# Kernel tuning notes

Hardware: AMD Instinct MI355X
Metric: run time of the kernel (lower is better)

Reference implementation:

```python
import jax, jax.numpy as jnp
import numpy as np

N_NODES = 50000
N_EDGES = 800000
H = 128   # atom_hidden_feats
B = 64    # bond_in_feats
NEG_SLOPE = 0.01  # torch LeakyReLU default


def setup_inputs() -> dict:
    key = jax.random.key(0)
    k1, k2, k3, k4, k5 = jax.random.split(key, 5)
    feat = jax.random.normal(k1, (N_NODES, H), dtype=jnp.float32)
    gdf_feat = jax.random.normal(k2, (N_EDGES, B), dtype=jnp.float32)
    # Linear(2H+B -> H): weight [H, 2H+B], bias [H]
    W = jax.random.normal(k3, (H, 2 * H + B), dtype=jnp.float32) * 0.05
    b = jnp.zeros((H,), dtype=jnp.float32)
    src = jax.random.randint(k4, (N_EDGES,), 0, N_NODES, dtype=jnp.int64)
    dst = jax.random.randint(k5, (N_EDGES,), 0, N_NODES, dtype=jnp.int64)
    return {"feat": feat, "gdf_feat": gdf_feat, "W": W, "b": b, "src": src, "dst": dst}


def reference(feat, gdf_feat, W, b, src, dst):
    n_nodes = feat.shape[0]
    # Per-edge message: concat(src_feat, dst_feat, edge_feat) -> linear -> gate
    z = jnp.concatenate([feat[src], feat[dst], gdf_feat], axis=-1)  # [E, 2H+B]
    z = z @ W.T + b                                                 # [E, H]
    msg = jax.nn.sigmoid(z) * jnp.where(z > 0, z, NEG_SLOPE * z)    # sigmoid * leaky_relu
    # Scatter-sum messages to destination nodes
    return jax.ops.segment_sum(msg, dst, num_segments=n_nodes)      # [N, H]
```

## Files before the change

### kernel.cpp

```cpp
#include <hip/hip_runtime.h>
#include <hip/hip_bf16.h>

typedef __attribute__((ext_vector_type(8)))  short bf16x8;
typedef __attribute__((ext_vector_type(16))) float f32x16;
typedef __attribute__((ext_vector_type(4)))  float f32x4;
typedef __attribute__((ext_vector_type(2)))  __fp16 fp16x2;

#define NN 50000
#define EE 800000
#define HH 128
#define KK 320
#define NEG 0.01f
#define NTILES (EE / 64)
#define NBLK 768
#define ACC_BYTES ((size_t)NN * HH * 2)

__device__ __forceinline__ unsigned pack2(float a, float b) {
    unsigned short lo = __builtin_bit_cast(unsigned short, __float2bfloat16(a));
    unsigned short hi = __builtin_bit_cast(unsigned short, __float2bfloat16(b));
    return (unsigned)lo | ((unsigned)hi << 16);
}

__global__ __launch_bounds__(256) void featcvt_kernel(const float* __restrict__ feat,
                                                      ushort* __restrict__ featb)
{
    const int t = blockIdx.x * 256 + threadIdx.x;
    const float* p = feat + (long long)t * 8;
    f32x4 v0 = *(const f32x4*)p;
    f32x4 v1 = *(const f32x4*)(p + 4);
    int4 h;
    h.x = (int)pack2(v0[0], v0[1]); h.y = (int)pack2(v0[2], v0[3]);
    h.z = (int)pack2(v1[0], v1[1]); h.w = (int)pack2(v1[2], v1[3]);
    *(int4*)(featb + (long long)t * 8) = h;
}

__global__ __launch_bounds__(256, 3) void fused_pipe_kernel(
    const ushort* __restrict__ featb, const float* __restrict__ gdf,
    const float*  __restrict__ W,     const float* __restrict__ bias,
    const int*    __restrict__ src,   const int*   __restrict__ dst,
    __fp16* __restrict__ acc16)
{
    __shared__ char lds[64 * 640];
    __shared__ int  dsts[2][64];

    const int tid  = threadIdx.x;
    const int lane = tid & 63;
    const int wid  = tid >> 6;
    const int col  = wid * 32 + (lane & 31);
    const int khalf = lane >> 5;
    const int r = tid >> 2, q = tid & 3;

    bf16x8 Wb[20];
    {
        const float* wrow = W + col * KK + khalf * 8;
        #pragma unroll
        for (int k = 0; k < 20; k++) {
            f32x4 x0 = *(const f32x4*)(wrow + k * 16);
            f32x4 x1 = *(const f32x4*)(wrow + k * 16 + 4);
            union { bf16x8 v; unsigned u[4]; } t;
            t.u[0] = pack2(x0[0], x0[1]); t.u[1] = pack2(x0[2], x0[3]);
            t.u[2] = pack2(x1[0], x1[1]); t.u[3] = pack2(x1[2], x1[3]);
            Wb[k] = t.v;
        }
    }
    const float bv = bias[col];

    int4  sf[8];
    f32x4 sgv[4];
    int   dStage;

    auto issueLoads = [&](long long t, int s_i, int d_i) {
        const ushort* fs = featb + (long long)s_i * HH;
        const ushort* fd = featb + (long long)d_i * HH;
        const float*  ge = gdf + (t * 64 + r) * 64;
        #pragma unroll
        for (int i = 0; i < 8; i++) {
            const int c = q + i * 4;
            sf[i] = *(const int4*)((c < 16) ? (fs + c * 8) : (fd + (c - 16) * 8));
        }
        #pragma unroll
        for (int i = 0; i < 2; i++) {
            const int cg = q + i * 4;
            sgv[2 * i]     = *(const f32x4*)(ge + cg * 8);
            sgv[2 * i + 1] = *(const f32x4*)(ge + cg * 8 + 4);
        }
    };
    auto writeStage = [&](int buf) {
        const int xr = (r & 7) << 4;
        #pragma unroll
        for (int i = 0; i < 8; i++) {
            const int c = q + i * 4;
            *(int4*)(lds + r * 640 + ((c * 16) ^ xr)) = sf[i];
        }
        #pragma unroll
        for (int i = 0; i < 2; i++) {
            const int c = 32 + q + i * 4;
            int4 h;
            h.x = (int)pack2(sgv[2*i][0], sgv[2*i][1]);
            h.y = (int)pack2(sgv[2*i][2], sgv[2*i][3]);
            h.z = (int)pack2(sgv[2*i+1][0], sgv[2*i+1][1]);
            h.w = (int)pack2(sgv[2*i+1][2], sgv[2*i+1][3]);
            *(int4*)(lds + r * 640 + ((c * 16) ^ xr)) = h;
        }
        if (q == 0) dsts[buf][r] = dStage;
    };

    int tile = blockIdx.x;
    {
        int s0 = src[(long long)tile * 64 + r];
        int d0 = dst[(long long)tile * 64 + r];
        issueLoads(tile, s0, d0);
        dStage = d0;
    }
    int nt = tile + NBLK;
    int sN, dN;
    {
        const long long tc = (nt < NTILES) ? nt : 0;
        sN = src[tc * 64 + r]; dN = dst[tc * 64 + r];
    }
    writeStage(0);
    asm volatile("s_waitcnt lgkmcnt(0)" ::: "memory");
    __builtin_amdgcn_sched_barrier(0);
    __builtin_amdgcn_s_barrier();

    const int arow = lane & 31;
    const int xa   = (arow & 7) << 4;
    int cur = 0;

    while (true) {
        const bool hasNext = (nt < NTILES);
        if (hasNext) {
            issueLoads(nt, sN, dN);
            dStage = dN;
            const long long tc = (nt + NBLK < NTILES) ? (long long)(nt + NBLK) : 0;
            sN = src[tc * 64 + r]; dN = dst[tc * 64 + r];
        }

        f32x16 acc0 = {}; f32x16 acc1 = {};
        #pragma unroll
        for (int k = 0; k < 20; k++) {
            const int kb = k * 32 + khalf * 16;
            bf16x8 a0 = *(const bf16x8*)(lds + arow * 640 + (kb ^ xa));
            bf16x8 a1 = *(const bf16x8*)(lds + (arow + 32) * 640 + (kb ^ xa));
            acc0 = __builtin_amdgcn_mfma_f32_32x32x16_bf16(a0, Wb[k], acc0, 0, 0, 0);
            acc1 = __builtin_amdgcn_mfma_f32_32x32x16_bf16(a1, Wb[k], acc1, 0, 0, 0);
        }

        if (hasNext) {
            __builtin_amdgcn_s_barrier();
            __builtin_amdgcn_sched_barrier(0);
            writeStage(cur ^ 1);
            asm volatile("s_waitcnt lgkmcnt(0)" ::: "memory");
            __builtin_amdgcn_sched_barrier(0);
            __builtin_amdgcn_s_barrier();
        }

        #pragma unroll
        for (int rt = 0; rt < 2; rt++) {
            const f32x16 A = rt ? acc1 : acc0;
            #pragma unroll
            for (int g = 0; g < 4; g++) {
                const int4 dn4 = *(const int4*)(&dsts[cur][rt * 32 + g * 8 + khalf * 4]);
                #pragma unroll
                for (int j = 0; j < 4; j++) {
                    const int reg = g * 4 + j;
                    const float z  = A[reg] + bv;
                    const float lr = z > 0.f ? z : NEG * z;
                    const float sgm = 1.f / (1.f + __expf(-z));
                    const float m  = lr * sgm;
                    const float o  = __shfl_xor(m, 1);
                    const int dn = ((const int*)&dn4)[j];
                    if (!(lane & 1)) {
                        fp16x2 hv = __builtin_amdgcn_cvt_pkrtz(m, o);
                        __fp16* p = acc16 + (long long)dn * HH + col;
                        asm volatile("global_atomic_pk_add_f16 %0, %1, off"
                                     :: "v"(p), "v"(hv) : "memory");
                    }
                }
            }
        }

        if (!hasNext) break;
        cur ^= 1; tile = nt; nt += NBLK;
    }
}

__global__ __launch_bounds__(256) void fused_fallback_kernel(
    const float* __restrict__ feat, const float* __restrict__ gdf,
    const float* __restrict__ W,    const float* __restrict__ bias,
    const int*   __restrict__ src,  const int*   __restrict__ dst,
    float* __restrict__ out)
{
    __shared__ int4 lds4[64 * 40];
    __shared__ int  dsts[64];
    char* lds = (char*)lds4;
    const int tid = threadIdx.x, lane = tid & 63, wid = tid >> 6;
    const int col = wid * 32 + (lane & 31), khalf = lane >> 5;
    const int r = tid >> 2, q = tid & 3;
    const long long ebase = (long long)blockIdx.x * 64;

    bf16x8 Wb[20];
    {
        const float* wrow = W + col * KK + khalf * 8;
        #pragma unroll
        for (int k = 0; k < 20; k++) {
            f32x4 x0 = *(const f32x4*)(wrow + k * 16);
            f32x4 x1 = *(const f32x4*)(wrow + k * 16 + 4);
            union { bf16x8 v; unsigned u[4]; } t;
            t.u[0] = pack2(x0[0], x0[1]); t.u[1] = pack2(x0[2], x0[3]);
            t.u[2] = pack2(x1[0], x1[1]); t.u[3] = pack2(x1[2], x1[3]);
            Wb[k] = t.v;
        }
    }
    const int s = src[ebase + r], d = dst[ebase + r];
    if (q == 0) dsts[r] = d;
    {
        const float* fs = feat + (long long)s * HH;
        const float* fd = feat + (long long)d * HH;
        const float* ge = gdf + (ebase + r) * 64;
        #pragma unroll
        for (int i = 0; i < 10; i++) {
            const int c = q + i * 4;
            const float* p = (c < 16) ? (fs + c * 8)
                           : (c < 32) ? (fd + (c - 16) * 8)
                                      : (ge + (c - 32) * 8);
            f32x4 v0 = *(const f32x4*)p;
            f32x4 v1 = *(const f32x4*)(p + 4);
            int4 h;
            h.x = (int)pack2(v0[0], v0[1]); h.y = (int)pack2(v0[2], v0[3]);
            h.z = (int)pack2(v1[0], v1[1]); h.w = (int)pack2(v1[2], v1[3]);
            *(int4*)(lds + r * 640 + ((c * 16) ^ ((r & 7) << 4))) = h;
        }
    }
    __syncthreads();
    f32x16 acc0 = {}; f32x16 acc1 = {};
    const int arow = lane & 31, xa = (arow & 7) << 4;
    #pragma unroll
    for (int k = 0; k < 20; k++) {
        const int kb = k * 32 + khalf * 16;
        bf16x8 a0 = *(const bf16x8*)(lds + arow * 640 + (kb ^ xa));
        bf16x8 a1 = *(const bf16x8*)(lds + (arow + 32) * 640 + (kb ^ xa));
        acc0 = __builtin_amdgcn_mfma_f32_32x32x16_bf16(a0, Wb[k], acc0, 0, 0, 0);
        acc1 = __builtin_amdgcn_mfma_f32_32x32x16_bf16(a1, Wb[k], acc1, 0, 0, 0);
    }
    const float bv = bias[col];
    #pragma unroll
    for (int rt = 0; rt < 2; rt++) {
        const f32x16 A = rt ? acc1 : acc0;
        #pragma unroll
        for (int g = 0; g < 4; g++) {
            #pragma unroll
            for (int j = 0; j < 4; j++) {
                const int reg = g * 4 + j;
                const int row = j + g * 8 + khalf * 4;
                const float z  = A[reg] + bv;
                const float lr = z > 0.f ? z : NEG * z;
                const float sgm = 1.f / (1.f + __expf(-z));
                unsafeAtomicAdd(out + (long long)dsts[rt * 32 + row] * HH + col, lr * sgm);
            }
        }
    }
}

__global__ __launch_bounds__(256) void conv_kernel(const int4* __restrict__ acc,
                                                   float4* __restrict__ out)
{
    const int i = blockIdx.x * 256 + threadIdx.x;
    union { int4 v; __fp16 h[8]; } u;
    u.v = acc[i];
    float4 a, b;
    a.x = (float)u.h[0]; a.y = (float)u.h[1]; a.z = (float)u.h[2]; a.w = (float)u.h[3];
    b.x = (float)u.h[4]; b.y = (float)u.h[5]; b.z = (float)u.h[6]; b.w = (float)u.h[7];
    out[2 * i]     = a;
    out[2 * i + 1] = b;
}

extern "C" void kernel_launch(void* const* d_in, const int* in_sizes, int n_in,
                              void* d_out, int out_size, void* d_ws, size_t ws_size,
                              hipStream_t stream) {
    const float* feat = (const float*)d_in[0];
    const float* gdf  = (const float*)d_in[1];
    const float* W    = (const float*)d_in[2];
    const float* bias = (const float*)d_in[3];
    const int*   src  = (const int*)d_in[4];
    const int*   dst  = (const int*)d_in[5];
    float* out = (float*)d_out;

    __fp16* acc16 = (__fp16*)d_ws;
    ushort* featb = (ushort*)((char*)d_ws + ACC_BYTES);

    if (ws_size >= 2 * ACC_BYTES) {
        (void)hipMemsetAsync(d_ws, 0, ACC_BYTES, stream);
        featcvt_kernel<<<NN * HH / 8 / 256, 256, 0, stream>>>(feat, featb);
        fused_pipe_kernel<<<NBLK, 256, 0, stream>>>(featb, gdf, W, bias,
                                                    src, dst, acc16);
        conv_kernel<<<NN * HH / 8 / 256, 256, 0, stream>>>((const int4*)d_ws,
                                                           (float4*)out);
    } else {
        (void)hipMemsetAsync(out, 0, (size_t)out_size * sizeof(float), stream);
        fused_fallback_kernel<<<EE / 64, 256, 0, stream>>>(feat, gdf, W, bias,
                                                           src, dst, out);
    }
}
```

Measured before the change: 371.2 us.

## Replace atomic scatter with counting-sort slots and segmented reduction

Builds a destination histogram, prefix scan and per-edge slot assignment, so each edge's fp16 message is written to a unique slot in a dst-sorted buffer instead of being atomically added. A separate reduce kernel then sums each node's contiguous messages into fp32 output. This removes global packed fp16 atomics and the conversion pass. In exchange it needs about 200MB of workspace, several extra kernel launches, and extra message write/read traffic. If the workspace is too small it falls back to the old atomic path.

```diff
diff --git a/kernel.cpp b/kernel.cpp
--- a/kernel.cpp
+++ b/kernel.cpp
@@ -13,7 +13,13 @@
 #define NEG 0.01f
 #define NTILES (EE / 64)
 #define NBLK 768
-#define ACC_BYTES ((size_t)NN * HH * 2)
+#define NSB 196
+
+#define MSG_BYTES   ((size_t)EE * HH * 2)
+#define FEATB_BYTES ((size_t)NN * HH * 2)
+#define SLOT_BYTES  ((size_t)EE * 4)
+#define CNT_BYTES   ((size_t)50176 * 4)
+#define ACC_BYTES   ((size_t)NN * HH * 2)
 
 __device__ __forceinline__ unsigned pack2(float a, float b) {
     unsigned short lo = __builtin_bit_cast(unsigned short, __float2bfloat16(a));
@@ -34,14 +40,75 @@
     *(int4*)(featb + (long long)t * 8) = h;
 }
 
-__global__ __launch_bounds__(256, 3) void fused_pipe_kernel(
+__global__ __launch_bounds__(256) void hist_kernel(const int* __restrict__ dst,
+                                                   unsigned* __restrict__ cnt)
+{
+    const int e = blockIdx.x * 256 + threadIdx.x;
+    atomicAdd(&cnt[dst[e]], 1u);
+}
+
+__global__ __launch_bounds__(256) void scan1_kernel(const unsigned* __restrict__ cnt,
+                                                    unsigned* __restrict__ base,
+                                                    unsigned* __restrict__ bsum)
+{
+    __shared__ unsigned s[256];
+    const int tid = threadIdx.x;
+    const int g = blockIdx.x * 256 + tid;
+    unsigned v = (g < NN) ? cnt[g] : 0u;
+    s[tid] = v; __syncthreads();
+    #pragma unroll
+    for (int o = 1; o < 256; o <<= 1) {
+        unsigned t = (tid >= o) ? s[tid - o] : 0u;
+        __syncthreads();
+        if (tid >= o) s[tid] += t;
+        __syncthreads();
+    }
+    if (g < NN) base[g] = s[tid] - v;
+    if (tid == 255) bsum[blockIdx.x] = s[255];
+}
+
+__global__ __launch_bounds__(256) void scan2_kernel(unsigned* __restrict__ bsum)
+{
+    __shared__ unsigned s[256];
+    const int tid = threadIdx.x;
+    unsigned v = (tid < NSB) ? bsum[tid] : 0u;
+    s[tid] = v; __syncthreads();
+    #pragma unroll
+    for (int o = 1; o < 256; o <<= 1) {
+        unsigned t = (tid >= o) ? s[tid - o] : 0u;
+        __syncthreads();
+        if (tid >= o) s[tid] += t;
+        __syncthreads();
+    }
+    if (tid < NSB) bsum[tid] = s[tid] - v;
+}
+
+__global__ __launch_bounds__(256) void scan3_kernel(unsigned* __restrict__ base,
+                                                    const unsigned* __restrict__ bsum)
+{
+    const int g = blockIdx.x * 256 + threadIdx.x;
+    if (g < NN) base[g] += bsum[blockIdx.x];
+}
+
+__global__ __launch_bounds__(256) void slot_kernel(const int* __restrict__ dst,
+                                                   const unsigned* __restrict__ base,
+                                                   unsigned* __restrict__ cursor,
+                                                   int* __restrict__ slot)
+{
+    const int e = blockIdx.x * 256 + threadIdx.x;
+    const int d = dst[e];
+    const unsigned rank = atomicAdd(&cursor[d], 1u);
+    slot[e] = (int)(base[d] + rank);
+}
+
+__global__ __launch_bounds__(256, 3) void fused_store_kernel(
     const ushort* __restrict__ featb, const float* __restrict__ gdf,
     const float*  __restrict__ W,     const float* __restrict__ bias,
     const int*    __restrict__ src,   const int*   __restrict__ dst,
-    __fp16* __restrict__ acc16)
+    const int*    __restrict__ slot,  __fp16* __restrict__ msg)
 {
     __shared__ char lds[64 * 640];
-    __shared__ int  dsts[2][64];
+    __shared__ int  sslot[2][64];
 
     const int tid  = threadIdx.x;
     const int lane = tid & 63;
@@ -67,7 +134,7 @@
 
     int4  sf[8];
     f32x4 sgv[4];
-    int   dStage;
+    int   slStage;
 
     auto issueLoads = [&](long long t, int s_i, int d_i) {
         const ushort* fs = featb + (long long)s_i * HH;
@@ -102,6 +169,174 @@
             h.w = (int)pack2(sgv[2*i+1][2], sgv[2*i+1][3]);
             *(int4*)(lds + r * 640 + ((c * 16) ^ xr)) = h;
         }
+        if (q == 0) sslot[buf][r] = slStage;
+    };
+
+    int tile = blockIdx.x;
+    {
+        int s0 = src[(long long)tile * 64 + r];
+        int d0 = dst[(long long)tile * 64 + r];
+        issueLoads(tile, s0, d0);
+        slStage = slot[(long long)tile * 64 + r];
+    }
+    int nt = tile + NBLK;
+    int sN, dN, slN;
+    {
+        const long long tc = (nt < NTILES) ? nt : 0;
+        sN = src[tc * 64 + r]; dN = dst[tc * 64 + r]; slN = slot[tc * 64 + r];
+    }
+    writeStage(0);
+    asm volatile("s_waitcnt lgkmcnt(0)" ::: "memory");
+    __builtin_amdgcn_sched_barrier(0);
+    __builtin_amdgcn_s_barrier();
+
+    const int arow = lane & 31;
+    const int xa   = (arow & 7) << 4;
+    int cur = 0;
+
+    while (true) {
+        const bool hasNext = (nt < NTILES);
+        if (hasNext) {
+            issueLoads(nt, sN, dN);
+            slStage = slN;
+            const long long tc = (nt + NBLK < NTILES) ? (long long)(nt + NBLK) : 0;
+            sN = src[tc * 64 + r]; dN = dst[tc * 64 + r]; slN = slot[tc * 64 + r];
+        }
+
+        f32x16 acc0 = {}; f32x16 acc1 = {};
+        #pragma unroll
+        for (int k = 0; k < 20; k++) {
+            const int kb = k * 32 + khalf * 16;
+            bf16x8 a0 = *(const bf16x8*)(lds + arow * 640 + (kb ^ xa));
+            bf16x8 a1 = *(const bf16x8*)(lds + (arow + 32) * 640 + (kb ^ xa));
+            acc0 = __builtin_amdgcn_mfma_f32_32x32x16_bf16(a0, Wb[k], acc0, 0, 0, 0);
+            acc1 = __builtin_amdgcn_mfma_f32_32x32x16_bf16(a1, Wb[k], acc1, 0, 0, 0);
+        }
+
+        if (hasNext) {
+            __builtin_amdgcn_s_barrier();
+            __builtin_amdgcn_sched_barrier(0);
+            writeStage(cur ^ 1);
+            asm volatile("s_waitcnt lgkmcnt(0)" ::: "memory");
+            __builtin_amdgcn_sched_barrier(0);
+            __builtin_amdgcn_s_barrier();
+        }
+
+        #pragma unroll
+        for (int rt = 0; rt < 2; rt++) {
+            const f32x16 A = rt ? acc1 : acc0;
+            #pragma unroll
+            for (int g = 0; g < 4; g++) {
+                const int4 sl4 = *(const int4*)(&sslot[cur][rt * 32 + g * 8 + khalf * 4]);
+                #pragma unroll
+                for (int j = 0; j < 4; j++) {
+                    const int reg = g * 4 + j;
+                    const float z  = A[reg] + bv;
+                    const float lr = z > 0.f ? z : NEG * z;
+                    const float sgm = 1.f / (1.f + __expf(-z));
+                    const float m  = lr * sgm;
+                    const float o  = __shfl_xor(m, 1);
+                    const int sl = ((const int*)&sl4)[j];
+                    if (!(lane & 1)) {
+                        fp16x2 hv = __builtin_amdgcn_cvt_pkrtz(m, o);
+                        *(fp16x2*)(msg + (long long)sl * HH + col) = hv;
+                    }
+                }
+            }
+        }
+
+        if (!hasNext) break;
+        cur ^= 1; tile = nt; nt += NBLK;
+    }
+}
+
+__global__ __launch_bounds__(256) void reduce_kernel(const __fp16* __restrict__ msg,
+                                                     const unsigned* __restrict__ base,
+                                                     const unsigned* __restrict__ cnt,
+                                                     float* __restrict__ out)
+{
+    const int n    = blockIdx.x * 4 + (threadIdx.x >> 6);
+    const int lane = threadIdx.x & 63;
+    const unsigned st  = base[n];
+    const unsigned deg = cnt[n];
+    float a0 = 0.f, a1 = 0.f;
+    unsigned j = 0;
+    union { unsigned u; __fp16 h[2]; } w0, w1;
+    for (; j + 2 <= deg; j += 2) {
+        w0.u = *(const unsigned*)(msg + ((long long)(st + j)     * HH) + lane * 2);
+        w1.u = *(const unsigned*)(msg + ((long long)(st + j + 1) * HH) + lane * 2);
+        a0 += (float)w0.h[0] + (float)w1.h[0];
+        a1 += (float)w0.h[1] + (float)w1.h[1];
+    }
+    if (j < deg) {
+        w0.u = *(const unsigned*)(msg + ((long long)(st + j) * HH) + lane * 2);
+        a0 += (float)w0.h[0];
+        a1 += (float)w0.h[1];
+    }
+    *(float2*)(out + (long long)n * HH + lane * 2) = float2{a0, a1};
+}
+
+__global__ __launch_bounds__(256, 3) void fused_pipe_kernel(
+    const ushort* __restrict__ featb, const float* __restrict__ gdf,
+    const float*  __restrict__ W,     const float* __restrict__ bias,
+    const int*    __restrict__ src,   const int*   __restrict__ dst,
+    __fp16* __restrict__ acc16)
+{
+    __shared__ char lds[64 * 640];
+    __shared__ int  dsts[2][64];
+    const int tid = threadIdx.x, lane = tid & 63, wid = tid >> 6;
+    const int col = wid * 32 + (lane & 31), khalf = lane >> 5;
+    const int r = tid >> 2, q = tid & 3;
+
+    bf16x8 Wb[20];
+    {
+        const float* wrow = W + col * KK + khalf * 8;
+        #pragma unroll
+        for (int k = 0; k < 20; k++) {
+            f32x4 x0 = *(const f32x4*)(wrow + k * 16);
+            f32x4 x1 = *(const f32x4*)(wrow + k * 16 + 4);
+            union { bf16x8 v; unsigned u[4]; } t;
+            t.u[0] = pack2(x0[0], x0[1]); t.u[1] = pack2(x0[2], x0[3]);
+            t.u[2] = pack2(x1[0], x1[1]); t.u[3] = pack2(x1[2], x1[3]);
+            Wb[k] = t.v;
+        }
+    }
+    const float bv = bias[col];
+    int4 sf[8]; f32x4 sgv[4]; int dStage;
+
+    auto issueLoads = [&](long long t, int s_i, int d_i) {
+        const ushort* fs = featb + (long long)s_i * HH;
+        const ushort* fd = featb + (long long)d_i * HH;
+        const float*  ge = gdf + (t * 64 + r) * 64;
+        #pragma unroll
+        for (int i = 0; i < 8; i++) {
+            const int c = q + i * 4;
+            sf[i] = *(const int4*)((c < 16) ? (fs + c * 8) : (fd + (c - 16) * 8));
+        }
+        #pragma unroll
+        for (int i = 0; i < 2; i++) {
+            const int cg = q + i * 4;
+            sgv[2 * i]     = *(const f32x4*)(ge + cg * 8);
+            sgv[2 * i + 1] = *(const f32x4*)(ge + cg * 8 + 4);
+        }
+    };
+    auto writeStage = [&](int buf) {
+        const int xr = (r & 7) << 4;
+        #pragma unroll
+        for (int i = 0; i < 8; i++) {
+            const int c = q + i * 4;
+            *(int4*)(lds + r * 640 + ((c * 16) ^ xr)) = sf[i];
+        }
+        #pragma unroll
+        for (int i = 0; i < 2; i++) {
+            const int c = 32 + q + i * 4;
+            int4 h;
+            h.x = (int)pack2(sgv[2*i][0], sgv[2*i][1]);
+            h.y = (int)pack2(sgv[2*i][2], sgv[2*i][3]);
+            h.z = (int)pack2(sgv[2*i+1][0], sgv[2*i+1][1]);
+            h.w = (int)pack2(sgv[2*i+1][2], sgv[2*i+1][3]);
+            *(int4*)(lds + r * 640 + ((c * 16) ^ xr)) = h;
+        }
         if (q == 0) dsts[buf][r] = dStage;
     };
 
@@ -123,10 +358,8 @@
     __builtin_amdgcn_sched_barrier(0);
     __builtin_amdgcn_s_barrier();
 
-    const int arow = lane & 31;
-    const int xa   = (arow & 7) << 4;
+    const int arow = lane & 31, xa = (arow & 7) << 4;
     int cur = 0;
-
     while (true) {
         const bool hasNext = (nt < NTILES);
         if (hasNext) {
@@ -135,7 +368,6 @@
             const long long tc = (nt + NBLK < NTILES) ? (long long)(nt + NBLK) : 0;
             sN = src[tc * 64 + r]; dN = dst[tc * 64 + r];
         }
-
         f32x16 acc0 = {}; f32x16 acc1 = {};
         #pragma unroll
         for (int k = 0; k < 20; k++) {
@@ -145,7 +377,6 @@
             acc0 = __builtin_amdgcn_mfma_f32_32x32x16_bf16(a0, Wb[k], acc0, 0, 0, 0);
             acc1 = __builtin_amdgcn_mfma_f32_32x32x16_bf16(a1, Wb[k], acc1, 0, 0, 0);
         }
-
         if (hasNext) {
             __builtin_amdgcn_s_barrier();
             __builtin_amdgcn_sched_barrier(0);
@@ -154,7 +385,6 @@
             __builtin_amdgcn_sched_barrier(0);
             __builtin_amdgcn_s_barrier();
         }
-
         #pragma unroll
         for (int rt = 0; rt < 2; rt++) {
             const f32x16 A = rt ? acc1 : acc0;
@@ -179,10 +409,22 @@
                 }
             }
         }
-
         if (!hasNext) break;
         cur ^= 1; tile = nt; nt += NBLK;
     }
+}
+
+__global__ __launch_bounds__(256) void conv_kernel(const int4* __restrict__ acc,
+                                                   float4* __restrict__ out)
+{
+    const int i = blockIdx.x * 256 + threadIdx.x;
+    union { int4 v; __fp16 h[8]; } u;
+    u.v = acc[i];
+    float4 a, b;
+    a.x = (float)u.h[0]; a.y = (float)u.h[1]; a.z = (float)u.h[2]; a.w = (float)u.h[3];
+    b.x = (float)u.h[4]; b.y = (float)u.h[5]; b.z = (float)u.h[6]; b.w = (float)u.h[7];
+    out[2 * i]     = a;
+    out[2 * i + 1] = b;
 }
 
 __global__ __launch_bounds__(256) void fused_fallback_kernel(
@@ -262,19 +504,6 @@
     }
 }
 
-__global__ __launch_bounds__(256) void conv_kernel(const int4* __restrict__ acc,
-                                                   float4* __restrict__ out)
-{
-    const int i = blockIdx.x * 256 + threadIdx.x;
-    union { int4 v; __fp16 h[8]; } u;
-    u.v = acc[i];
-    float4 a, b;
-    a.x = (float)u.h[0]; a.y = (float)u.h[1]; a.z = (float)u.h[2]; a.w = (float)u.h[3];
-    b.x = (float)u.h[4]; b.y = (float)u.h[5]; b.z = (float)u.h[6]; b.w = (float)u.h[7];
-    out[2 * i]     = a;
-    out[2 * i + 1] = b;
-}
-
 extern "C" void kernel_launch(void* const* d_in, const int* in_sizes, int n_in,
                               void* d_out, int out_size, void* d_ws, size_t ws_size,
                               hipStream_t stream) {
@@ -286,13 +515,33 @@
     const int*   dst  = (const int*)d_in[5];
     float* out = (float*)d_out;
 
-    __fp16* acc16 = (__fp16*)d_ws;
-    ushort* featb = (ushort*)((char*)d_ws + ACC_BYTES);
-
-    if (ws_size >= 2 * ACC_BYTES) {
+    char* wsb = (char*)d_ws;
+    __fp16*   msg    = (__fp16*)wsb;
+    ushort*   featb  = (ushort*)(wsb + MSG_BYTES);
+    int*      slot   = (int*)(wsb + MSG_BYTES + FEATB_BYTES);
+    unsigned* cnt    = (unsigned*)(wsb + MSG_BYTES + FEATB_BYTES + SLOT_BYTES);
+    unsigned* base   = cnt + 50176;
+    unsigned* cursor = base + 50176;
+    unsigned* bsum   = cursor + 50176;
+    const size_t fullBytes = MSG_BYTES + FEATB_BYTES + SLOT_BYTES + 3 * CNT_BYTES + 1024;
+
+    if (ws_size >= fullBytes) {
+        (void)hipMemsetAsync(cnt, 0, 3 * CNT_BYTES + 1024, stream);
+        featcvt_kernel<<<NN * HH / 8 / 256, 256, 0, stream>>>(feat, featb);
+        hist_kernel<<<EE / 256, 256, 0, stream>>>(dst, cnt);
+        scan1_kernel<<<NSB, 256, 0, stream>>>(cnt, base, bsum);
+        scan2_kernel<<<1, 256, 0, stream>>>(bsum);
+        scan3_kernel<<<NSB, 256, 0, stream>>>(base, bsum);
+        slot_kernel<<<EE / 256, 256, 0, stream>>>(dst, base, cursor, slot);
+        fused_store_kernel<<<NBLK, 256, 0, stream>>>(featb, gdf, W, bias,
+                                                     src, dst, slot, msg);
+        reduce_kernel<<<NN / 4, 256, 0, stream>>>(msg, base, cnt, out);
+    } else if (ws_size >= 2 * ACC_BYTES) {
+        __fp16* acc16 = (__fp16*)d_ws;
+        ushort* fb2   = (ushort*)(wsb + ACC_BYTES);
         (void)hipMemsetAsync(d_ws, 0, ACC_BYTES, stream);
-        featcvt_kernel<<<NN * HH / 8 / 256, 256, 0, stream>>>(feat, featb);
-        fused_pipe_kernel<<<NBLK, 256, 0, stream>>>(featb, gdf, W, bias,
+        featcvt_kernel<<<NN * HH / 8 / 256, 256, 0, stream>>>(feat, fb2);
+        fused_pipe_kernel<<<NBLK, 256, 0, stream>>>(fb2, gdf, W, bias,
                                                     src, dst, acc16);
         conv_kernel<<<NN * HH / 8 / 256, 256, 0, stream>>>((const int4*)d_ws,
                                                            (float4*)out);
```

Measured after the change: 506.0 us. 1.36x slower.

## Sort edges by destination and pre-combine same-destination messages before atomics

Applied to the files above, without the earlier changes.

Adds a counting sort of edges by destination (histogram, three-stage scan, atomic permutation build). The main kernel walks contiguous sorted tile ranges per block, with XCD-aware block-to-range mapping, and sums runs of equal destinations in registers before issuing packed fp16 atomics. The aim is fewer atomics and better locality for the destination-feature gather and the scatter. In exchange it adds several preprocessing kernels per call, an indirect gather of gdf through the permutation, and it drops the register double-buffered prefetch pipeline, so loads are now synchronous with the compute.

```diff
diff --git a/kernel.cpp b/kernel.cpp
--- a/kernel.cpp
+++ b/kernel.cpp
@@ -13,7 +13,12 @@
 #define NEG 0.01f
 #define NTILES (EE / 64)
 #define NBLK 768
-#define ACC_BYTES ((size_t)NN * HH * 2)
+#define NSB 196
+
+#define ACC_BYTES   ((size_t)NN * HH * 2)
+#define FEATB_BYTES ((size_t)NN * HH * 2)
+#define PERM_BYTES  ((size_t)EE * 4)
+#define CNT_BYTES   ((size_t)50176 * 4)
 
 __device__ __forceinline__ unsigned pack2(float a, float b) {
     unsigned short lo = __builtin_bit_cast(unsigned short, __float2bfloat16(a));
@@ -34,14 +39,75 @@
     *(int4*)(featb + (long long)t * 8) = h;
 }
 
-__global__ __launch_bounds__(256, 3) void fused_pipe_kernel(
+__global__ __launch_bounds__(256) void hist_kernel(const int* __restrict__ dst,
+                                                   unsigned* __restrict__ cnt)
+{
+    const int e = blockIdx.x * 256 + threadIdx.x;
+    atomicAdd(&cnt[dst[e]], 1u);
+}
+
+__global__ __launch_bounds__(256) void scan1_kernel(const unsigned* __restrict__ cnt,
+                                                    unsigned* __restrict__ base,
+                                                    unsigned* __restrict__ bsum)
+{
+    __shared__ unsigned s[256];
+    const int tid = threadIdx.x;
+    const int g = blockIdx.x * 256 + tid;
+    unsigned v = (g < NN) ? cnt[g] : 0u;
+    s[tid] = v; __syncthreads();
+    #pragma unroll
+    for (int o = 1; o < 256; o <<= 1) {
+        unsigned t = (tid >= o) ? s[tid - o] : 0u;
+        __syncthreads();
+        if (tid >= o) s[tid] += t;
+        __syncthreads();
+    }
+    if (g < NN) base[g] = s[tid] - v;
+    if (tid == 255) bsum[blockIdx.x] = s[255];
+}
+
+__global__ __launch_bounds__(256) void scan2_kernel(unsigned* __restrict__ bsum)
+{
+    __shared__ unsigned s[256];
+    const int tid = threadIdx.x;
+    unsigned v = (tid < NSB) ? bsum[tid] : 0u;
+    s[tid] = v; __syncthreads();
+    #pragma unroll
+    for (int o = 1; o < 256; o <<= 1) {
+        unsigned t = (tid >= o) ? s[tid - o] : 0u;
+        __syncthreads();
+        if (tid >= o) s[tid] += t;
+        __syncthreads();
+    }
+    if (tid < NSB) bsum[tid] = s[tid] - v;
+}
+
+__global__ __launch_bounds__(256) void scan3_kernel(unsigned* __restrict__ base,
+                                                    const unsigned* __restrict__ bsum)
+{
+    const int g = blockIdx.x * 256 + threadIdx.x;
+    if (g < NN) base[g] += bsum[blockIdx.x];
+}
+
+__global__ __launch_bounds__(256) void permbuild_kernel(const int* __restrict__ dst,
+                                                        const unsigned* __restrict__ base,
+                                                        unsigned* __restrict__ cursor,
+                                                        int* __restrict__ perm)
+{
+    const int e = blockIdx.x * 256 + threadIdx.x;
+    const int d = dst[e];
+    const unsigned rank = atomicAdd(&cursor[d], 1u);
+    perm[base[d] + rank] = e;
+}
+
+__global__ __launch_bounds__(256, 3) void fused_sorted_kernel(
     const ushort* __restrict__ featb, const float* __restrict__ gdf,
     const float*  __restrict__ W,     const float* __restrict__ bias,
     const int*    __restrict__ src,   const int*   __restrict__ dst,
-    __fp16* __restrict__ acc16)
+    const int*    __restrict__ perm,  __fp16* __restrict__ acc16)
 {
     __shared__ char lds[64 * 640];
-    __shared__ int  dsts[2][64];
+    __shared__ int  dsts[64];
 
     const int tid  = threadIdx.x;
     const int lane = tid & 63;
@@ -65,76 +131,62 @@
     }
     const float bv = bias[col];
 
-    int4  sf[8];
-    f32x4 sgv[4];
-    int   dStage;
-
-    auto issueLoads = [&](long long t, int s_i, int d_i) {
-        const ushort* fs = featb + (long long)s_i * HH;
-        const ushort* fd = featb + (long long)d_i * HH;
-        const float*  ge = gdf + (t * 64 + r) * 64;
-        #pragma unroll
-        for (int i = 0; i < 8; i++) {
-            const int c = q + i * 4;
-            sf[i] = *(const int4*)((c < 16) ? (fs + c * 8) : (fd + (c - 16) * 8));
-        }
-        #pragma unroll
-        for (int i = 0; i < 2; i++) {
-            const int cg = q + i * 4;
-            sgv[2 * i]     = *(const f32x4*)(ge + cg * 8);
-            sgv[2 * i + 1] = *(const f32x4*)(ge + cg * 8 + 4);
-        }
-    };
-    auto writeStage = [&](int buf) {
-        const int xr = (r & 7) << 4;
-        #pragma unroll
-        for (int i = 0; i < 8; i++) {
-            const int c = q + i * 4;
-            *(int4*)(lds + r * 640 + ((c * 16) ^ xr)) = sf[i];
-        }
-        #pragma unroll
-        for (int i = 0; i < 2; i++) {
-            const int c = 32 + q + i * 4;
-            int4 h;
-            h.x = (int)pack2(sgv[2*i][0], sgv[2*i][1]);
-            h.y = (int)pack2(sgv[2*i][2], sgv[2*i][3]);
-            h.z = (int)pack2(sgv[2*i+1][0], sgv[2*i+1][1]);
-            h.w = (int)pack2(sgv[2*i+1][2], sgv[2*i+1][3]);
-            *(int4*)(lds + r * 640 + ((c * 16) ^ xr)) = h;
-        }
-        if (q == 0) dsts[buf][r] = dStage;
-    };
-
-    int tile = blockIdx.x;
+    const int xcd = blockIdx.x & 7, wI = blockIdx.x >> 3;
+    const int cid = xcd * (NBLK / 8) + wI;
+    const int qc  = NTILES / NBLK;
+    const int rem = NTILES % NBLK;
+    const int t0  = cid * qc + (cid < rem ? cid : rem);
+    const int len = qc + (cid < rem ? 1 : 0);
+
+    int eCur, sCur, dCur;
     {
-        int s0 = src[(long long)tile * 64 + r];
-        int d0 = dst[(long long)tile * 64 + r];
-        issueLoads(tile, s0, d0);
-        dStage = d0;
-    }
-    int nt = tile + NBLK;
-    int sN, dN;
-    {
-        const long long tc = (nt < NTILES) ? nt : 0;
-        sN = src[tc * 64 + r]; dN = dst[tc * 64 + r];
-    }
-    writeStage(0);
-    asm volatile("s_waitcnt lgkmcnt(0)" ::: "memory");
-    __builtin_amdgcn_sched_barrier(0);
-    __builtin_amdgcn_s_barrier();
+        const long long p = (long long)t0 * 64 + r;
+        eCur = perm[p]; sCur = src[eCur]; dCur = dst[eCur];
+    }
 
     const int arow = lane & 31;
     const int xa   = (arow & 7) << 4;
-    int cur = 0;
-
-    while (true) {
-        const bool hasNext = (nt < NTILES);
-        if (hasNext) {
-            issueLoads(nt, sN, dN);
-            dStage = dN;
-            const long long tc = (nt + NBLK < NTILES) ? (long long)(nt + NBLK) : 0;
-            sN = src[tc * 64 + r]; dN = dst[tc * 64 + r];
-        }
+
+    auto flush = [&](int dn, float v) {
+        const float o = __shfl_xor(v, 1);
+        if (!(lane & 1)) {
+            fp16x2 hv = __builtin_amdgcn_cvt_pkrtz(v, o);
+            __fp16* pa = acc16 + (long long)dn * HH + col;
+            asm volatile("global_atomic_pk_add_f16 %0, %1, off"
+                         :: "v"(pa), "v"(hv) : "memory");
+        }
+    };
+
+    for (int t = t0; t < t0 + len; ++t) {
+        if (q == 0) dsts[r] = dCur;
+        {
+            const ushort* fs = featb + (long long)sCur * HH;
+            const ushort* fd = featb + (long long)dCur * HH;
+            const float*  ge = gdf + (long long)eCur * 64;
+            const int xr = (r & 7) << 4;
+            #pragma unroll
+            for (int i = 0; i < 8; i++) {
+                const int c = q + i * 4;
+                int4 h = *(const int4*)((c < 16) ? (fs + c * 8) : (fd + (c - 16) * 8));
+                *(int4*)(lds + r * 640 + ((c * 16) ^ xr)) = h;
+            }
+            #pragma unroll
+            for (int i = 8; i < 10; i++) {
+                const int c = q + i * 4;
+                const float* p = ge + (c - 32) * 8;
+                f32x4 v0 = *(const f32x4*)p;
+                f32x4 v1 = *(const f32x4*)(p + 4);
+                int4 h;
+                h.x = (int)pack2(v0[0], v0[1]); h.y = (int)pack2(v0[2], v0[3]);
+                h.z = (int)pack2(v1[0], v1[1]); h.w = (int)pack2(v1[2], v1[3]);
+                *(int4*)(lds + r * 640 + ((c * 16) ^ xr)) = h;
+            }
+        }
+        if (t + 1 < t0 + len) {
+            const long long p = (long long)(t + 1) * 64 + r;
+            eCur = perm[p]; sCur = src[eCur]; dCur = dst[eCur];
+        }
+        __syncthreads();
 
         f32x16 acc0 = {}; f32x16 acc1 = {};
         #pragma unroll
@@ -146,43 +198,44 @@
             acc1 = __builtin_amdgcn_mfma_f32_32x32x16_bf16(a1, Wb[k], acc1, 0, 0, 0);
         }
 
-        if (hasNext) {
-            __builtin_amdgcn_s_barrier();
-            __builtin_amdgcn_sched_barrier(0);
-            writeStage(cur ^ 1);
-            asm volatile("s_waitcnt lgkmcnt(0)" ::: "memory");
-            __builtin_amdgcn_sched_barrier(0);
-            __builtin_amdgcn_s_barrier();
-        }
-
         #pragma unroll
         for (int rt = 0; rt < 2; rt++) {
             const f32x16 A = rt ? acc1 : acc0;
             #pragma unroll
             for (int g = 0; g < 4; g++) {
-                const int4 dn4 = *(const int4*)(&dsts[cur][rt * 32 + g * 8 + khalf * 4]);
+                const int4 dn4 = *(const int4*)(&dsts[rt * 32 + g * 8 + khalf * 4]);
+                const int dd[4] = { dn4.x, dn4.y, dn4.z, dn4.w };
+                float mm[4];
                 #pragma unroll
                 for (int j = 0; j < 4; j++) {
-                    const int reg = g * 4 + j;
-                    const float z  = A[reg] + bv;
+                    const float z  = A[g * 4 + j] + bv;
                     const float lr = z > 0.f ? z : NEG * z;
-                    const float sgm = 1.f / (1.f + __expf(-z));
-                    const float m  = lr * sgm;
-                    const float o  = __shfl_xor(m, 1);
-                    const int dn = ((const int*)&dn4)[j];
-                    if (!(lane & 1)) {
-                        fp16x2 hv = __builtin_amdgcn_cvt_pkrtz(m, o);
-                        __fp16* p = acc16 + (long long)dn * HH + col;
-                        asm volatile("global_atomic_pk_add_f16 %0, %1, off"
-                                     :: "v"(p), "v"(hv) : "memory");
-                    }
+                    mm[j] = lr / (1.f + __expf(-z));
                 }
+                float s = mm[0];
+                #pragma unroll
+                for (int j = 1; j < 4; j++) {
+                    if (dd[j] == dd[j - 1]) s += mm[j];
+                    else { flush(dd[j - 1], s); s = mm[j]; }
+                }
+                flush(dd[3], s);
             }
         }
-
-        if (!hasNext) break;
-        cur ^= 1; tile = nt; nt += NBLK;
-    }
+        __syncthreads();
+    }
+}
+
+__global__ __launch_bounds__(256) void conv_kernel(const int4* __restrict__ acc,
+                                                   float4* __restrict__ out)
+{
+    const int i = blockIdx.x * 256 + threadIdx.x;
+    union { int4 v; __fp16 h[8]; } u;
+    u.v = acc[i];
+    float4 a, b;
+    a.x = (float)u.h[0]; a.y = (float)u.h[1]; a.z = (float)u.h[2]; a.w = (float)u.h[3];
+    b.x = (float)u.h[4]; b.y = (float)u.h[5]; b.z = (float)u.h[6]; b.w = (float)u.h[7];
+    out[2 * i]     = a;
+    out[2 * i + 1] = b;
 }
 
 __global__ __launch_bounds__(256) void fused_fallback_kernel(
@@ -262,19 +315,6 @@
     }
 }
 
-__global__ __launch_bounds__(256) void conv_kernel(const int4* __restrict__ acc,
-                                                   float4* __restrict__ out)
-{
-    const int i = blockIdx.x * 256 + threadIdx.x;
-    union { int4 v; __fp16 h[8]; } u;
-    u.v = acc[i];
-    float4 a, b;
-    a.x = (float)u.h[0]; a.y = (float)u.h[1]; a.z = (float)u.h[2]; a.w = (float)u.h[3];
-    b.x = (float)u.h[4]; b.y = (float)u.h[5]; b.z = (float)u.h[6]; b.w = (float)u.h[7];
-    out[2 * i]     = a;
-    out[2 * i + 1] = b;
-}
-
 extern "C" void kernel_launch(void* const* d_in, const int* in_sizes, int n_in,
                               void* d_out, int out_size, void* d_ws, size_t ws_size,
                               hipStream_t stream) {
@@ -286,15 +326,29 @@
     const int*   dst  = (const int*)d_in[5];
     float* out = (float*)d_out;
 
-    __fp16* acc16 = (__fp16*)d_ws;
-    ushort* featb = (ushort*)((char*)d_ws + ACC_BYTES);
-
-    if (ws_size >= 2 * ACC_BYTES) {
-        (void)hipMemsetAsync(d_ws, 0, ACC_BYTES, stream);
+    char* wsb = (char*)d_ws;
+    __fp16*   acc16  = (__fp16*)wsb;
+    ushort*   featb  = (ushort*)(wsb + ACC_BYTES);
+    int*      perm   = (int*)(wsb + ACC_BYTES + FEATB_BYTES);
+    unsigned* cnt    = (unsigned*)(wsb + ACC_BYTES + FEATB_BYTES + PERM_BYTES);
+    unsigned* base   = cnt + 50176;
+    unsigned* cursor = base + 50176;
+    unsigned* bsum   = cursor + 50176;
+    const size_t fullBytes = ACC_BYTES + FEATB_BYTES + PERM_BYTES + 3 * CNT_BYTES + 4096;
+
+    if (ws_size >= fullBytes) {
+        (void)hipMemsetAsync(acc16, 0, ACC_BYTES, stream);
+        (void)hipMemsetAsync(cnt, 0, CNT_BYTES, stream);
+        (void)hipMemsetAsync(cursor, 0, CNT_BYTES + 4096, stream);
         featcvt_kernel<<<NN * HH / 8 / 256, 256, 0, stream>>>(feat, featb);
-        fused_pipe_kernel<<<NBLK, 256, 0, stream>>>(featb, gdf, W, bias,
-                                                    src, dst, acc16);
-        conv_kernel<<<NN * HH / 8 / 256, 256, 0, stream>>>((const int4*)d_ws,
+        hist_kernel<<<EE / 256, 256, 0, stream>>>(dst, cnt);
+        scan1_kernel<<<NSB, 256, 0, stream>>>(cnt, base, bsum);
+        scan2_kernel<<<1, 256, 0, stream>>>(bsum);
+        scan3_kernel<<<NSB, 256, 0, stream>>>(base, bsum);
+        permbuild_kernel<<<EE / 256, 256, 0, stream>>>(dst, base, cursor, perm);
+        fused_sorted_kernel<<<NBLK, 256, 0, stream>>>(featb, gdf, W, bias,
+                                                      src, dst, perm, acc16);
+        conv_kernel<<<NN * HH / 8 / 256, 256, 0, stream>>>((const int4*)acc16,
                                                            (float4*)out);
     } else {
         (void)hipMemsetAsync(out, 0, (size_t)out_size * sizeof(float), stream);
```

Result: faster. 359.9 us (-3.1%).
